# Optimization experiments

Measured on AMD Instinct MI355X. Metric: run time of the kernel, lower is better.

The kernel has to match this reference:

```python
import jax, jax.numpy as jnp
import numpy as np

U = 4        # num_users
B = 64       # batch
N = 2048     # n_antennas (RIS elements)
F = 4        # feature_dim per user
H = 16       # local_info_dim + global_info_dim
LD = 8       # local_info_dim
GD = 8       # global_info_dim
CIN = F + 2 * H  # 36, input channels for layers 2-7 and final conv


def setup_inputs() -> dict:
    key = jax.random.key(0)
    ks = jax.random.split(key, 12)
    w = lambda k, s: (jax.random.normal(k, s, dtype=jnp.float32) * 0.1)
    return {
        "channel": jax.random.normal(ks[0], (B, U * F, N), dtype=jnp.float32),
        "We1": w(ks[1], (H, F)), "be1": w(ks[2], (H,)),
        "We": w(ks[3], (6, H, CIN)), "be": w(ks[4], (6, H)),
        "Wo1": w(ks[5], (H, F)), "bo1": w(ks[6], (H,)),
        "Wo": w(ks[7], (6, H, CIN)), "bo": w(ks[8], (6, H)),
        "W8": w(ks[9], (1, CIN)), "b8": w(ks[10], (1,)),
        "num_users": U,
    }


def _conv1x1(f, W, b):
    # f: [U, B, Cin, N], W: [Cout, Cin] -> [U, B, Cout, N]
    return jnp.einsum('ubcn,oc->ubon', f, W) + b[None, None, :, None]


def _forward(channel, We1, be1, We, be, Wo1, bo1, Wo, bo, W8, b8, num_users):
    b_, nf, n = channel.shape
    fpu = nf // num_users
    # split per-user channel slices -> [U, B, F, N]
    ch = channel.reshape(b_, num_users, fpu, n).transpose(1, 0, 2, 3)
    feats = ch
    for i in range(7):
        We_i = We1 if i == 0 else We[i - 1]
        be_i = be1 if i == 0 else be[i - 1]
        Wo_i = Wo1 if i == 0 else Wo[i - 1]
        bo_i = bo1 if i == 0 else bo[i - 1]
        ego = jax.nn.relu(_conv1x1(feats, We_i, be_i))       # [U,B,H,N]
        opp = jax.nn.relu(_conv1x1(feats, Wo_i, bo_i))       # [U,B,H,N]
        # leave-one-out mean over users: sum-then-subtract (O(U) not O(U^2))
        loo = (jnp.sum(opp, axis=0, keepdims=True) - opp) / (num_users - 1)

        def split(o):
            g = jnp.mean(o[:, :, -GD:, :], axis=3, keepdims=True)
            g = jnp.broadcast_to(g, (num_users, b_, GD, n))
            return o[:, :, :LD, :], g

        el, eg = split(ego)
        ol, og = split(loo)
        feats = jnp.concatenate([ch, el, eg, ol, og], axis=2)  # [U,B,36,N]
    fm = jnp.mean(feats, axis=0)                              # [B,36,N]
    out = (jnp.einsum('bcn,oc->bon', fm, W8) + b8[None, :, None]) * jnp.float32(np.pi)
    return out  # [B,1,N]


def reference(channel, We1, be1, We, be, Wo1, bo1, Wo, bo, W8, b8, num_users):
    return _forward(channel, We1, be1, We, be, Wo1, bo1, Wo, bo, W8, b8, num_users)
```

## Files before the change

### kernel.cpp

```cpp
#include <hip/hip_runtime.h>
#include <hip/hip_cooperative_groups.h>

namespace cg = cooperative_groups;

#define TPB 1024
#define GRID 256


typedef float f2 __attribute__((ext_vector_type(2)));
static __device__ __forceinline__ f2 spl(float s) { f2 r; r.x = s; r.y = s; return r; }

__global__ void risnet_kernel(
    const float* __restrict__ channel,
    const float* __restrict__ We1, const float* __restrict__ be1,
    const float* __restrict__ We,  const float* __restrict__ be,
    const float* __restrict__ Wo1, const float* __restrict__ bo1,
    const float* __restrict__ Wo,  const float* __restrict__ bo,
    const float* __restrict__ W8,  const float* __restrict__ b8,
    float* __restrict__ out, float* __restrict__ part, int* __restrict__ gcnt)
{
  const int tid   = threadIdx.x;
  const int lane  = tid & 63;
  const int wv    = tid >> 6;
  const int p     = tid & 1;
  const int B     = blockIdx.x;
  const int b     = (B & 7) * 8 + ((B >> 3) & 7);
  const int chunk = B >> 6;
  const int n     = (chunk << 9) | (tid >> 1);

  __shared__ __align__(16) float biasE[2][16][4];
  __shared__ __align__(16) float biasO[2][16][4];
  __shared__ float red[64][64];
  __shared__ float gv[64];
  __shared__ float fin;

  f2 ch2[4];
#pragma unroll
  for (int f = 0; f < 4; ++f) {
    ch2[f].x = channel[((b*4 + 2*p + 0)*4 + f)*2048 + n];
    ch2[f].y = channel[((b*4 + 2*p + 1)*4 + f)*2048 + n];
  }

  f2 el2[8], ol2[8];

#define BFLY3(a0, a1) { \
  a0 += __shfl_xor(a0, 2, 64);  a1 += __shfl_xor(a1, 2, 64);  \
  a0 += __shfl_xor(a0, 4, 64);  a1 += __shfl_xor(a1, 4, 64);  \
  a0 += __shfl_xor(a0, 8, 64);  a1 += __shfl_xor(a1, 8, 64); }

#define RED_W(base_col, a0, a1) \
  if ((lane & 15) < 2) { \
    red[(wv<<2)|(lane>>4)][(base_col) + 2*(lane&1) + 0] = a0; \
    red[(wv<<2)|(lane>>4)][(base_col) + 2*(lane&1) + 1] = a1; }

#define PUBLISH(Lpar) { \
  __syncthreads(); \
  if (tid < 64) { \
    float s0 = 0.f, s1 = 0.f, s2 = 0.f, s3 = 0.f; \
    _Pragma("unroll") for (int r = 0; r < 64; r += 4) { \
      s0 += red[r+0][tid]; s1 += red[r+1][tid]; \
      s2 += red[r+2][tid]; s3 += red[r+3][tid]; \
    } \
    __hip_atomic_store(&part[(((Lpar)*64 + b)*4 + chunk)*64 + tid], \
                       (s0+s1)+(s2+s3), \
                       __ATOMIC_RELAXED, __HIP_MEMORY_SCOPE_AGENT); \
    asm volatile("s_waitcnt vmcnt(0)" ::: "memory"); \
    if (lane == 0) \
      __hip_atomic_fetch_add(&gcnt[b], 1, __ATOMIC_RELAXED, __HIP_MEMORY_SCOPE_AGENT); \
  } }

#define SPIN_CNT(tgt) { \
  for (;;) { \
    int c = __hip_atomic_load(&gcnt[b], __ATOMIC_RELAXED, __HIP_MEMORY_SCOPE_AGENT); \
    if (c >= (tgt)) break; \
    __builtin_amdgcn_s_sleep(1); \
  } \
  asm volatile("" ::: "memory"); }

#define DOT20B(ACC, W0, W1, W2, W5, W6, BINIT) { \
  f2 v = (BINIT); \
  v = spl(W0.x)*ch2[0] + v; v = spl(W0.y)*ch2[1] + v; \
  v = spl(W0.z)*ch2[2] + v; v = spl(W0.w)*ch2[3] + v; \
  v = spl(W1.x)*el2[0] + v; v = spl(W1.y)*el2[1] + v; \
  v = spl(W1.z)*el2[2] + v; v = spl(W1.w)*el2[3] + v; \
  v = spl(W2.x)*el2[4] + v; v = spl(W2.y)*el2[5] + v; \
  v = spl(W2.z)*el2[6] + v; v = spl(W2.w)*el2[7] + v; \
  v = spl(W5.x)*ol2[0] + v; v = spl(W5.y)*ol2[1] + v; \
  v = spl(W5.z)*ol2[2] + v; v = spl(W5.w)*ol2[3] + v; \
  v = spl(W6.x)*ol2[4] + v; v = spl(W6.y)*ol2[5] + v; \
  v = spl(W6.z)*ol2[6] + v; v = spl(W6.w)*ol2[7] + v; \
  ACC = v; }

  {
    f2 opl2[8];
#pragma unroll
    for (int h = 0; h < 16; ++h) {
      const float4 w = *(const float4*)(We1 + h*4);
      f2 a = spl(be1[h]);
      a = spl(w.x)*ch2[0] + a; a = spl(w.y)*ch2[1] + a;
      a = spl(w.z)*ch2[2] + a; a = spl(w.w)*ch2[3] + a;
      a.x = fmaxf(a.x, 0.f); a.y = fmaxf(a.y, 0.f);
      if (h < 8) el2[h] = a;
      else { float a0 = a.x, a1 = a.y; BFLY3(a0, a1); RED_W((h-8)*4, a0, a1); }
    }
#pragma unroll
    for (int h = 0; h < 16; ++h) {
      const float4 w = *(const float4*)(Wo1 + h*4);
      f2 a = spl(bo1[h]);
      a = spl(w.x)*ch2[0] + a; a = spl(w.y)*ch2[1] + a;
      a = spl(w.z)*ch2[2] + a; a = spl(w.w)*ch2[3] + a;
      a.x = fmaxf(a.x, 0.f); a.y = fmaxf(a.y, 0.f);
      if (h < 8) opl2[h] = a;
      else { float a0 = a.x, a1 = a.y; BFLY3(a0, a1); RED_W(32 + (h-8)*4, a0, a1); }
    }
#pragma unroll
    for (int j = 0; j < 8; ++j) {
      const float s2 = opl2[j].x + opl2[j].y;
      const float s4 = s2 + __shfl_xor(s2, 1, 64);
      ol2[j] = (spl(s4) - opl2[j]) * spl(1.f/3.f);
    }
  }
  PUBLISH(0)

  for (int L = 1; L < 7; ++L) {
    const float* __restrict__ wEl = We + (L-1)*576;
    const float* __restrict__ wOl = Wo + (L-1)*576;
    const int par_r = (L-1) & 1;
    const int par_w = L & 1;
    const int bb    = L & 1;

    f2 accE2[16];
#pragma unroll
    for (int h = 0; h < 16; ++h) {
      const float4* wr = (const float4*)(wEl + h*36);
      const float4 w0 = wr[0], w1 = wr[1], w2 = wr[2], w5 = wr[5], w6 = wr[6];
      DOT20B(accE2[h], w0, w1, w2, w5, w6, spl(0.f))
    }

    if (wv == 15) {
      SPIN_CNT(4*L)
      float s = 0.f;
#pragma unroll
      for (int k = 0; k < 4; ++k)
        s += __hip_atomic_load(&part[((par_r*64 + b)*4 + k)*64 + lane],
                               __ATOMIC_RELAXED, __HIP_MEMORY_SCOPE_AGENT);
      gv[lane] = s * (1.f/2048.f);
      const int u = lane & 3;
      const int h = lane >> 2;
      float bE = be[(L-1)*16 + h];
      float bO = bo[(L-1)*16 + h];
#pragma unroll
      for (int j = 0; j < 8; ++j) {
        const float eg = gv[j*4 + u];
        const float so = gv[32+j*4+0] + gv[32+j*4+1] + gv[32+j*4+2] + gv[32+j*4+3];
        const float og = (so - gv[32 + j*4 + u]) * (1.f/3.f);
        bE += wEl[h*36 + 12 + j] * eg + wEl[h*36 + 28 + j] * og;
        bO += wOl[h*36 + 12 + j] * eg + wOl[h*36 + 28 + j] * og;
      }
      biasE[bb][h][u] = bE;
      biasO[bb][h][u] = bO;
    }
    __syncthreads();

#pragma unroll
    for (int h = 8; h < 16; ++h) {
      f2 a = accE2[h] + *(const f2*)&biasE[bb][h][2*p];
      float a0 = fmaxf(a.x, 0.f), a1 = fmaxf(a.y, 0.f);
      BFLY3(a0, a1); RED_W((h-8)*4, a0, a1);
    }
#pragma unroll
    for (int h = 8; h < 16; ++h) {
      const float4* wr = (const float4*)(wOl + h*36);
      const float4 w0 = wr[0], w1 = wr[1], w2 = wr[2], w5 = wr[5], w6 = wr[6];
      f2 a;
      DOT20B(a, w0, w1, w2, w5, w6, *(const f2*)&biasO[bb][h][2*p])
      float a0 = fmaxf(a.x, 0.f), a1 = fmaxf(a.y, 0.f);
      BFLY3(a0, a1); RED_W(32 + (h-8)*4, a0, a1);
    }
    PUBLISH(par_w)

    f2 eln2[8];
#pragma unroll
    for (int h = 0; h < 8; ++h) {
      f2 a = accE2[h] + *(const f2*)&biasE[bb][h][2*p];
      a.x = fmaxf(a.x, 0.f); a.y = fmaxf(a.y, 0.f);
      eln2[h] = a;
    }
    f2 opl2[8];
#pragma unroll
    for (int h = 0; h < 8; ++h) {
      const float4* wr = (const float4*)(wOl + h*36);
      const float4 w0 = wr[0], w1 = wr[1], w2 = wr[2], w5 = wr[5], w6 = wr[6];
      f2 a;
      DOT20B(a, w0, w1, w2, w5, w6, *(const f2*)&biasO[bb][h][2*p])
      a.x = fmaxf(a.x, 0.f); a.y = fmaxf(a.y, 0.f);
      opl2[h] = a;
    }
#pragma unroll
    for (int j = 0; j < 8; ++j) {
      const float s2 = opl2[j].x + opl2[j].y;
      const float s4 = s2 + __shfl_xor(s2, 1, 64);
      ol2[j] = (spl(s4) - opl2[j]) * spl(1.f/3.f);
      el2[j] = eln2[j];
    }
  }

  if (wv == 0) {
    SPIN_CNT(28)
    float s = 0.f;
#pragma unroll
    for (int k = 0; k < 4; ++k)
      s += __hip_atomic_load(&part[((0*64 + b)*4 + k)*64 + lane],
                             __ATOMIC_RELAXED, __HIP_MEMORY_SCOPE_AGENT);
    gv[lane] = s * (1.f/2048.f);
    if (lane == 0) {
      float sf = b8[0];
#pragma unroll
      for (int j = 0; j < 8; ++j) {
        const float so = gv[32+j*4+0] + gv[32+j*4+1] + gv[32+j*4+2] + gv[32+j*4+3];
#pragma unroll
        for (int u = 0; u < 4; ++u) {
          const float eg = gv[j*4 + u];
          const float og = (so - gv[32 + j*4 + u]) * (1.f/3.f);
          sf += 0.25f * (W8[12 + j] * eg + W8[28 + j] * og);
        }
      }
      fin = sf;
    }
  }
  __syncthreads();
  f2 v = spl(0.f);
#pragma unroll
  for (int c = 0; c < 4; ++c) v = spl(W8[c]) * ch2[c] + v;
#pragma unroll
  for (int j = 0; j < 8; ++j) {
    v = spl(W8[4 + j]) * el2[j] + v;
    v = spl(W8[20 + j]) * ol2[j] + v;
  }
  float t = v.x + v.y;
  t += __shfl_xor(t, 1, 64);
  if (p == 0)
    out[b*2048 + n] = (fin + 0.25f * t) * 3.14159265358979f;
}

extern "C" void kernel_launch(void* const* d_in, const int* in_sizes, int n_in,
                              void* d_out, int out_size, void* d_ws, size_t ws_size,
                              hipStream_t stream) {
  const float* channel = (const float*)d_in[0];
  const float* We1 = (const float*)d_in[1];
  const float* be1 = (const float*)d_in[2];
  const float* We  = (const float*)d_in[3];
  const float* be  = (const float*)d_in[4];
  const float* Wo1 = (const float*)d_in[5];
  const float* bo1 = (const float*)d_in[6];
  const float* Wo  = (const float*)d_in[7];
  const float* bo  = (const float*)d_in[8];
  const float* W8  = (const float*)d_in[9];
  const float* b8  = (const float*)d_in[10];
  float* out  = (float*)d_out;
  float* part = (float*)d_ws;
  int*   gcnt = (int*)((char*)d_ws + 131072);

  hipMemsetAsync(gcnt, 0, 64 * sizeof(int), stream);

  void* args[] = { (void*)&channel, (void*)&We1, (void*)&be1, (void*)&We, (void*)&be,
                   (void*)&Wo1, (void*)&bo1, (void*)&Wo, (void*)&bo,
                   (void*)&W8, (void*)&b8, (void*)&out, (void*)&part, (void*)&gcnt };
  hipLaunchCooperativeKernel((void*)risnet_kernel, dim3(GRID), dim3(TPB), args, 0, stream);
}
```

Before: 127.2 us.

## Replace block barrier in publish with wave counter and atomic-add partials

Removes the __syncthreads before each per-layer publish. Each wave now bumps a shared-memory counter, and only wave 0 waits for all 16 waves before reducing and publishing. Cross-block partials are accumulated with atomic adds into one running-sum slot per parity instead of four per-chunk slots, and readers subtract the previous cumulative value to get the per-layer sum. This aims to let waves proceed without a full block barrier and to cut the number of global loads per layer. The risks are floating-point cancellation from the cumulative subtraction and a larger workspace memset.

```diff
diff --git a/kernel.cpp b/kernel.cpp
--- a/kernel.cpp
+++ b/kernel.cpp
@@ -1,7 +1,5 @@
 #include <hip/hip_runtime.h>
 #include <hip/hip_cooperative_groups.h>
-
-namespace cg = cooperative_groups;
 
 #define TPB 1024
 #define GRID 256
@@ -33,6 +31,9 @@
   __shared__ float red[64][64];
   __shared__ float gv[64];
   __shared__ float fin;
+  __shared__ int   lcnt;
+
+  if (tid == 0) lcnt = 0;
 
   f2 ch2[4];
 #pragma unroll
@@ -40,8 +41,11 @@
     ch2[f].x = channel[((b*4 + 2*p + 0)*4 + f)*2048 + n];
     ch2[f].y = channel[((b*4 + 2*p + 1)*4 + f)*2048 + n];
   }
+  __syncthreads();
 
   f2 el2[8], ol2[8];
+  float cum0 = 0.f, cum1 = 0.f;
+  int   pubt = 16;
 
 #define BFLY3(a0, a1) { \
   a0 += __shfl_xor(a0, 2, 64);  a1 += __shfl_xor(a1, 2, 64);  \
@@ -53,21 +57,30 @@
     red[(wv<<2)|(lane>>4)][(base_col) + 2*(lane&1) + 0] = a0; \
     red[(wv<<2)|(lane>>4)][(base_col) + 2*(lane&1) + 1] = a1; }
 
-#define PUBLISH(Lpar) { \
-  __syncthreads(); \
-  if (tid < 64) { \
+#define WAVE_DONE() { \
+  asm volatile("s_waitcnt lgkmcnt(0)" ::: "memory"); \
+  if (lane == 0) \
+    __hip_atomic_fetch_add(&lcnt, 1, __ATOMIC_RELAXED, __HIP_MEMORY_SCOPE_WORKGROUP); }
+
+#define PUBLISH_W0(par) \
+  if (wv == 0) { \
+    for (;;) { \
+      int c = __hip_atomic_load(&lcnt, __ATOMIC_RELAXED, __HIP_MEMORY_SCOPE_WORKGROUP); \
+      if (c >= pubt) break; \
+      __builtin_amdgcn_s_sleep(0); \
+    } \
+    asm volatile("" ::: "memory"); \
     float s0 = 0.f, s1 = 0.f, s2 = 0.f, s3 = 0.f; \
     _Pragma("unroll") for (int r = 0; r < 64; r += 4) { \
-      s0 += red[r+0][tid]; s1 += red[r+1][tid]; \
-      s2 += red[r+2][tid]; s3 += red[r+3][tid]; \
+      s0 += red[r+0][lane]; s1 += red[r+1][lane]; \
+      s2 += red[r+2][lane]; s3 += red[r+3][lane]; \
     } \
-    __hip_atomic_store(&part[(((Lpar)*64 + b)*4 + chunk)*64 + tid], \
-                       (s0+s1)+(s2+s3), \
-                       __ATOMIC_RELAXED, __HIP_MEMORY_SCOPE_AGENT); \
+    unsafeAtomicAdd(&part[((par)*64 + b)*64 + lane], (s0+s1)+(s2+s3)); \
     asm volatile("s_waitcnt vmcnt(0)" ::: "memory"); \
     if (lane == 0) \
       __hip_atomic_fetch_add(&gcnt[b], 1, __ATOMIC_RELAXED, __HIP_MEMORY_SCOPE_AGENT); \
-  } }
+  } \
+  pubt += 16;
 
 #define SPIN_CNT(tgt) { \
   for (;;) { \
@@ -113,6 +126,8 @@
       if (h < 8) opl2[h] = a;
       else { float a0 = a.x, a1 = a.y; BFLY3(a0, a1); RED_W(32 + (h-8)*4, a0, a1); }
     }
+    WAVE_DONE()
+    PUBLISH_W0(0)
 #pragma unroll
     for (int j = 0; j < 8; ++j) {
       const float s2 = opl2[j].x + opl2[j].y;
@@ -120,14 +135,13 @@
       ol2[j] = (spl(s4) - opl2[j]) * spl(1.f/3.f);
     }
   }
-  PUBLISH(0)
 
   for (int L = 1; L < 7; ++L) {
     const float* __restrict__ wEl = We + (L-1)*576;
     const float* __restrict__ wOl = Wo + (L-1)*576;
-    const int par_r = (L-1) & 1;
-    const int par_w = L & 1;
-    const int bb    = L & 1;
+    const int pr = (L-1) & 1;
+    const int pw = L & 1;
+    const int bb = L & 1;
 
     f2 accE2[16];
 #pragma unroll
@@ -139,12 +153,12 @@
 
     if (wv == 15) {
       SPIN_CNT(4*L)
-      float s = 0.f;
-#pragma unroll
-      for (int k = 0; k < 4; ++k)
-        s += __hip_atomic_load(&part[((par_r*64 + b)*4 + k)*64 + lane],
-                               __ATOMIC_RELAXED, __HIP_MEMORY_SCOPE_AGENT);
-      gv[lane] = s * (1.f/2048.f);
+      float R = __hip_atomic_load(&part[(pr*64 + b)*64 + lane],
+                                  __ATOMIC_RELAXED, __HIP_MEMORY_SCOPE_AGENT);
+      float prev = pr ? cum1 : cum0;
+      float d = R - prev;
+      if (pr) cum1 = R; else cum0 = R;
+      gv[lane] = d * (1.f/2048.f);
       const int u = lane & 3;
       const int h = lane >> 2;
       float bE = be[(L-1)*16 + h];
@@ -177,7 +191,8 @@
       float a0 = fmaxf(a.x, 0.f), a1 = fmaxf(a.y, 0.f);
       BFLY3(a0, a1); RED_W(32 + (h-8)*4, a0, a1);
     }
-    PUBLISH(par_w)
+    WAVE_DONE()
+    PUBLISH_W0(pw)
 
     f2 eln2[8];
 #pragma unroll
@@ -205,14 +220,11 @@
     }
   }
 
-  if (wv == 0) {
+  if (wv == 15) {
     SPIN_CNT(28)
-    float s = 0.f;
-#pragma unroll
-    for (int k = 0; k < 4; ++k)
-      s += __hip_atomic_load(&part[((0*64 + b)*4 + k)*64 + lane],
-                             __ATOMIC_RELAXED, __HIP_MEMORY_SCOPE_AGENT);
-    gv[lane] = s * (1.f/2048.f);
+    float R = __hip_atomic_load(&part[(0*64 + b)*64 + lane],
+                                __ATOMIC_RELAXED, __HIP_MEMORY_SCOPE_AGENT);
+    gv[lane] = (R - cum0) * (1.f/2048.f);
     if (lane == 0) {
       float sf = b8[0];
 #pragma unroll
@@ -259,9 +271,9 @@
   const float* b8  = (const float*)d_in[10];
   float* out  = (float*)d_out;
   float* part = (float*)d_ws;
-  int*   gcnt = (int*)((char*)d_ws + 131072);
-
-  hipMemsetAsync(gcnt, 0, 64 * sizeof(int), stream);
+  int*   gcnt = (int*)((char*)d_ws + 32768);
+
+  hipMemsetAsync(d_ws, 0, 32768 + 64 * sizeof(int), stream);
 
   void* args[] = { (void*)&channel, (void*)&We1, (void*)&be1, (void*)&We, (void*)&be,
                    (void*)&Wo1, (void*)&bo1, (void*)&Wo, (void*)&bo,
```

Result: faster. 119.1 us (-6.3%).
